# Kernel optimization log

Hardware: AMD Instinct MI355X
Metric: run time of the kernel (lower is better)

## Reference

```python
import jax, jax.numpy as jnp
import numpy as np

NODES_PER_GRAPH = 57
NUM_BRANCHES = 80
NUM_GRAPHS = 4096
IN_CH = 4
HID = 128
NUM_LAYERS = 5
BN_EPS = 1e-5


def setup_inputs() -> dict:
    key = jax.random.key(0)
    ks = jax.random.split(key, 24)
    N = NUM_GRAPHS * NODES_PER_GRAPH
    E = NUM_GRAPHS * NUM_BRANCHES * 2  # bidirectional branches per graph
    x = jax.random.normal(ks[0], (N, IN_CH), dtype=jnp.float32)
    # within-graph random edges, offset per graph block
    ep = jax.random.randint(ks[1], (2, E), 0, NODES_PER_GRAPH, dtype=jnp.int32)
    off = jnp.repeat(jnp.arange(NUM_GRAPHS, dtype=jnp.int32) * NODES_PER_GRAPH,
                     NUM_BRANCHES * 2)
    edge_index = ep + off[None, :]
    i = np.arange(NUM_BRANCHES)
    branch_u = jnp.asarray(i % NODES_PER_GRAPH, dtype=jnp.int32)
    branch_v = jnp.asarray((i * 7 + 3) % NODES_PER_GRAPH, dtype=jnp.int32)
    s = 0.05
    return {
        "x": x, "edge_index": edge_index,
        "branch_u": branch_u, "branch_v": branch_v,
        "Wp": jax.random.normal(ks[2], (IN_CH, HID)) * s,
        "bp": jnp.zeros((HID,), jnp.float32),
        "conv_W": jax.random.normal(ks[3], (NUM_LAYERS, HID, HID)) * s,
        "conv_b": jnp.zeros((NUM_LAYERS, HID), jnp.float32),
        "bn_gamma": jnp.ones((NUM_LAYERS, HID), jnp.float32),
        "bn_beta": jnp.zeros((NUM_LAYERS, HID), jnp.float32),
        "bn_mean": jax.random.normal(ks[4], (NUM_LAYERS, HID)) * 0.1,
        "bn_var": jax.random.uniform(ks[5], (NUM_LAYERS, HID)) + 0.5,
        "phys_W1": jax.random.normal(ks[6], (HID, 16)) * s,
        "phys_b1": jnp.zeros((16,), jnp.float32),
        "phys_W2": jax.random.normal(ks[7], (16, 1)) * s,
        "phys_b2": jnp.zeros((1,), jnp.float32),
        "mlp_W1": jax.random.normal(ks[8], (2 * HID + 1, HID)) * s,
        "mlp_b1": jnp.zeros((HID,), jnp.float32),
        "mlp_W2": jax.random.normal(ks[9], (HID, 1)) * s,
        "mlp_b2": jnp.zeros((1,), jnp.float32),
    }


def _gcn_conv(x, edge_index, W, b, num_nodes):
    # PyG GCNConv: add self-loops, symmetric deg^{-1/2} normalization,
    # message = norm * (x @ W)[src], scatter-add into dst, then + bias.
    h = x @ W
    loop = jnp.arange(num_nodes, dtype=edge_index.dtype)
    src = jnp.concatenate([edge_index[0], loop])
    dst = jnp.concatenate([edge_index[1], loop])
    deg = jax.ops.segment_sum(jnp.ones_like(dst, dtype=h.dtype), dst,
                              num_segments=num_nodes)  # >= 1 (self-loop)
    dinv = jax.lax.rsqrt(deg)
    norm = dinv[src] * dinv[dst]  # [E+N]
    out = jax.ops.segment_sum(h[src] * norm[:, None], dst,
                              num_segments=num_nodes)
    return out + b


def _forward(x, edge_index, branch_u, branch_v, Wp, bp, conv_W, conv_b,
             bn_gamma, bn_beta, bn_mean, bn_var, phys_W1, phys_b1, phys_W2,
             phys_b2, mlp_W1, mlp_b1, mlp_W2, mlp_b2):
    N = x.shape[0]
    num_graphs = N // NODES_PER_GRAPH
    h = x @ Wp + bp
    for l in range(NUM_LAYERS):
        res = h
        h = _gcn_conv(h, edge_index, conv_W[l], conv_b[l], N)
        # BatchNorm1d in eval mode (running stats); dropout is identity in eval
        h = (h - bn_mean[l]) * jax.lax.rsqrt(bn_var[l] + BN_EPS) * bn_gamma[l] + bn_beta[l]
        h = jax.nn.relu(h)
        h = h + res
    theta = jax.nn.relu(h @ phys_W1 + phys_b1) @ phys_W2 + phys_b2  # [N,1]
    offsets = (jnp.arange(num_graphs, dtype=jnp.int32) * NODES_PER_GRAPH)
    u_idx = (branch_u[None, :] + offsets[:, None]).reshape(-1)
    v_idx = (branch_v[None, :] + offsets[:, None]).reshape(-1)
    edge_feat = jnp.concatenate([h[u_idx], h[v_idx]], axis=-1)  # [G*80, 2H]
    delta_theta = theta[u_idx] - theta[v_idx]                   # [G*80, 1]
    comb = jnp.concatenate([edge_feat, delta_theta], axis=-1)
    return jax.nn.relu(comb @ mlp_W1 + mlp_b1) @ mlp_W2 + mlp_b2


def reference(x, edge_index, branch_u, branch_v, Wp, bp, conv_W, conv_b,
              bn_gamma, bn_beta, bn_mean, bn_var, phys_W1, phys_b1, phys_W2,
              phys_b2, mlp_W1, mlp_b1, mlp_W2, mlp_b2):
    return _forward(x, edge_index, branch_u, branch_v, Wp, bp, conv_W, conv_b,
                    bn_gamma, bn_beta, bn_mean, bn_var, phys_W1, phys_b1,
                    phys_W2, phys_b2, mlp_W1, mlp_b1, mlp_W2, mlp_b2)
```

## Files before the change

kernel.cpp:

```cpp
#include <hip/hip_runtime.h>

#define NPG 57
#define NEPG 160
#define NB 80
#define HID 128
#define NG 4096
#define NL 5

typedef __attribute__((ext_vector_type(8))) _Float16 f16x8;
typedef __attribute__((ext_vector_type(4))) _Float16 f16x4;
typedef __attribute__((ext_vector_type(4))) float f32x4;

#define MFMA16(A, B, C) __builtin_amdgcn_mfma_f32_16x16x32_f16(A, B, C, 0, 0, 0)

__device__ __forceinline__ f16x8 ldf8(const _Float16* base, int byteoff) {
    return *(const f16x8*)((const char*)base + byteoff);
}

__global__ void prep(const float* __restrict__ convW, const float* __restrict__ mlpW1,
                     const float* __restrict__ physW1, const float* __restrict__ convb,
                     const float* __restrict__ bn_gamma, const float* __restrict__ bn_beta,
                     const float* __restrict__ bn_mean, const float* __restrict__ bn_var,
                     _Float16* __restrict__ wb, float* __restrict__ fsc,
                     float* __restrict__ fsh) {
    int id = blockIdx.x * 256 + threadIdx.x;
    if (id < 114688) {
        int mat = id >> 14, rem = id & 16383, n = rem >> 7, k = rem & 127;
        float w;
        if (mat < 5)       w = convW[mat * 16384 + k * 128 + n];
        else if (mat == 5) w = mlpW1[k * 128 + n];
        else               w = mlpW1[(128 + k) * 128 + n];
        _Float16 hi = (_Float16)w;
        wb[mat * 32768 + n * 128 + k] = hi;
        wb[mat * 32768 + 16384 + n * 128 + k] = (_Float16)(w - (float)hi);
    } else if (id < 116736) {
        int p = id - 114688, n = p >> 7, k = p & 127;
        float w = physW1[k * 16 + n];
        _Float16 hi = (_Float16)w;
        wb[229376 + p] = hi;
        wb[231424 + p] = (_Float16)(w - (float)hi);
    } else if (id < 117376) {
        int p = id - 116736;
        float sc = bn_gamma[p] * rsqrtf(bn_var[p] + 1e-5f);
        fsc[p] = sc;
        fsh[p] = fmaf(convb[p] - bn_mean[p], sc, bn_beta[p]);
    }
}

__global__ __launch_bounds__(512, 2) void pinn_fused(
    const float* __restrict__ x, const int* __restrict__ edge_index,
    const int* __restrict__ branch_u, const int* __restrict__ branch_v,
    const float* __restrict__ Wp, const float* __restrict__ bp,
    const float* __restrict__ physb1, const float* __restrict__ physW2,
    const float* __restrict__ physb2,
    const float* __restrict__ mlpW1, const float* __restrict__ mlpb1,
    const float* __restrict__ mlpW2, const float* __restrict__ mlpb2,
    const _Float16* __restrict__ wb, const float* __restrict__ fsc,
    const float* __restrict__ fsh, float* __restrict__ out) {
    __shared__ _Float16 hTh[128 * 64];
    __shared__ _Float16 hTl[128 * 64];
    __shared__ _Float16 mh[64 * 128];
    __shared__ _Float16 ml[64 * 128];
    __shared__ float dinv[64];
    __shared__ int   deg[64];
    __shared__ short esrc[NEPG], edst[NEPG];
    __shared__ float theta[64];
    __shared__ float red[NB];
    __shared__ int   bu[NB], bv[NB];

    const int g = blockIdx.x;
    const int tid = threadIdx.x;
    const int lane = tid & 63;
    const int wv = tid >> 6;
    const int ln15 = lane & 15;
    const int hi4 = lane >> 4;
    const int R0 = 16 * (wv & 3);
    const int ct0 = 4 * (wv >> 2);

    float* Af = (float*)mh;
    _Float16* Ah = ml;
    _Float16* Al = ml + 4096;

    {
        int c = tid & 127;
        int sw = (c & 7) << 4;
        float w0 = Wp[c], w1 = Wp[HID + c], w2 = Wp[2 * HID + c], w3 = Wp[3 * HID + c];
        float bb = bp[c];
        for (int r = tid >> 7; r < 64; r += 4) {
            float h0 = 0.f;
            if (r < NPG) {
                float4 xv = ((const float4*)x)[g * NPG + r];
                h0 = fmaf(xv.x, w0, fmaf(xv.y, w1, fmaf(xv.z, w2, fmaf(xv.w, w3, bb))));
            }
            _Float16 hh = (_Float16)h0;
            *(_Float16*)((char*)(hTh + c * 64) + ((r * 2) ^ sw)) = hh;
            *(_Float16*)((char*)(hTl + c * 64) + ((r * 2) ^ sw)) = (_Float16)(h0 - (float)hh);
        }
    }
    for (int i = tid; i < 4096; i += 512) Af[i] = 0.f;
    if (tid < 64) deg[tid] = (tid < NPG) ? 1 : 0;
    if (tid < NB) { bu[tid] = branch_u[tid]; bv[tid] = branch_v[tid]; red[tid] = 0.f; }
    __syncthreads();

    if (tid < NEPG) {
        int gs = edge_index[g * NEPG + tid];
        int gd = edge_index[NG * NEPG + g * NEPG + tid];
        esrc[tid] = (short)(gs - g * NPG);
        edst[tid] = (short)(gd - g * NPG);
        atomicAdd(&deg[edst[tid]], 1);
    }
    __syncthreads();
    if (tid < 64) dinv[tid] = (tid < NPG) ? rsqrtf((float)deg[tid]) : 0.f;
    __syncthreads();
    if (tid < NEPG) {
        int s = esrc[tid], d = edst[tid];
        atomicAdd(&Af[d * 64 + s], dinv[s] * dinv[d]);
    }
    if (tid < NPG) atomicAdd(&Af[tid * 64 + tid], dinv[tid] * dinv[tid]);
    __syncthreads();
    for (int i = tid; i < 4096; i += 512) {
        int r = i >> 6, s = i & 63;
        float v = Af[i];
        _Float16 hi = (_Float16)v;
        int byteoff = (s * 2) ^ ((r & 7) << 4);
        *(_Float16*)((char*)(Ah + r * 64) + byteoff) = hi;
        *(_Float16*)((char*)(Al + r * 64) + byteoff) = (_Float16)(v - (float)hi);
    }
    __syncthreads();

    f16x8 Ahf[2], Alf[2];
    {
        int ar = R0 + ln15;
        int swr = (ar & 7) << 4;
        Ahf[0] = ldf8(Ah + ar * 64, ((8 * hi4) * 2) ^ swr);
        Ahf[1] = ldf8(Ah + ar * 64, ((32 + 8 * hi4) * 2) ^ swr);
        Alf[0] = ldf8(Al + ar * 64, ((8 * hi4) * 2) ^ swr);
        Alf[1] = ldf8(Al + ar * 64, ((32 + 8 * hi4) * 2) ^ swr);
    }
    __syncthreads();

    const int mrow = R0 + ln15;
    const int swm = (mrow & 7) << 4;

    for (int l = 0; l < NL; ++l) {
        f32x4 macc[4];
#pragma unroll
        for (int j = 0; j < 4; ++j) macc[j] = (f32x4){0.f, 0.f, 0.f, 0.f};
#pragma unroll
        for (int ks2 = 0; ks2 < 2; ++ks2) {
#pragma unroll
            for (int j = 0; j < 4; ++j) {
                int c = 16 * (ct0 + j) + ln15;
                int byteoff = ((32 * ks2 + 8 * hi4) * 2) ^ ((c & 7) << 4);
                f16x8 hh = ldf8(hTh + c * 64, byteoff);
                f16x8 hl = ldf8(hTl + c * 64, byteoff);
                f32x4 a = macc[j];
                a = MFMA16(Ahf[ks2], hh, a);
                a = MFMA16(Ahf[ks2], hl, a);
                a = MFMA16(Alf[ks2], hh, a);
                macc[j] = a;
            }
        }
#pragma unroll
        for (int j = 0; j < 4; ++j) {
            int c = 16 * (ct0 + j) + ln15;
#pragma unroll
            for (int q = 0; q < 4; ++q) {
                int r = R0 + 4 * hi4 + q;
                float v = macc[j][q];
                _Float16 vh = (_Float16)v;
                int byteoff = (c * 2) ^ ((r & 7) << 4);
                *(_Float16*)((char*)(mh + r * 128) + byteoff) = vh;
                *(_Float16*)((char*)(ml + r * 128) + byteoff) = (_Float16)(v - (float)vh);
            }
        }
        __syncthreads();

        const _Float16* whi = wb + 2 * l * 16384;
        const _Float16* wlo = wb + (2 * l + 1) * 16384;
        f32x4 zacc[4];
#pragma unroll
        for (int j = 0; j < 4; ++j) zacc[j] = (f32x4){0.f, 0.f, 0.f, 0.f};
#pragma unroll
        for (int ks = 0; ks < 4; ++ks) {
            int byteoff = ((32 * ks + 8 * hi4) * 2) ^ swm;
            f16x8 mhf = ldf8(mh + mrow * 128, byteoff);
            f16x8 mlf = ldf8(ml + mrow * 128, byteoff);
#pragma unroll
            for (int j = 0; j < 4; ++j) {
                int n = 16 * (ct0 + j) + ln15;
                f16x8 bh = *(const f16x8*)(whi + n * 128 + 32 * ks + 8 * hi4);
                f16x8 bl = *(const f16x8*)(wlo + n * 128 + 32 * ks + 8 * hi4);
                f32x4 a = zacc[j];
                a = MFMA16(mhf, bh, a);
                a = MFMA16(mhf, bl, a);
                a = MFMA16(mlf, bh, a);
                zacc[j] = a;
            }
        }

        if (l < NL - 1) {
#pragma unroll
            for (int j = 0; j < 4; ++j) {
                int c = 16 * (ct0 + j) + ln15;
                float scv = fsc[l * HID + c], shv = fsh[l * HID + c];
                int byteoff = ((R0 + 4 * hi4) * 2) ^ ((c & 7) << 4);
                f16x4 rh = *(const f16x4*)((const char*)(hTh + c * 64) + byteoff);
                f16x4 rl = *(const f16x4*)((const char*)(hTl + c * 64) + byteoff);
                f16x4 nh, nl;
#pragma unroll
                for (int q = 0; q < 4; ++q) {
                    float hold = (float)rh[q] + (float)rl[q];
                    float hnew = fmaxf(fmaf(zacc[j][q], scv, shv), 0.f) + hold;
                    _Float16 vh = (_Float16)hnew;
                    nh[q] = vh;
                    nl[q] = (_Float16)(hnew - (float)vh);
                }
                *(f16x4*)((char*)(hTh + c * 64) + byteoff) = nh;
                *(f16x4*)((char*)(hTl + c * 64) + byteoff) = nl;
            }
            __syncthreads();
        } else {
            __syncthreads();
#pragma unroll
            for (int j = 0; j < 4; ++j) {
                int c = 16 * (ct0 + j) + ln15;
                float scv = fsc[l * HID + c], shv = fsh[l * HID + c];
                int tbyte = ((R0 + 4 * hi4) * 2) ^ ((c & 7) << 4);
                f16x4 rh = *(const f16x4*)((const char*)(hTh + c * 64) + tbyte);
                f16x4 rl = *(const f16x4*)((const char*)(hTl + c * 64) + tbyte);
#pragma unroll
                for (int q = 0; q < 4; ++q) {
                    int r = R0 + 4 * hi4 + q;
                    float hold = (float)rh[q] + (float)rl[q];
                    float hnew = fmaxf(fmaf(zacc[j][q], scv, shv), 0.f) + hold;
                    _Float16 vh = (_Float16)hnew;
                    int byteoff = (c * 2) ^ ((r & 7) << 4);
                    *(_Float16*)((char*)(mh + r * 128) + byteoff) = vh;
                    *(_Float16*)((char*)(ml + r * 128) + byteoff) = (_Float16)(hnew - (float)vh);
                }
            }
            __syncthreads();
        }
    }

    if (wv < 4) {
        f32x4 t4 = (f32x4){0.f, 0.f, 0.f, 0.f};
        int r = 16 * wv + ln15;
        int swr = (r & 7) << 4;
#pragma unroll
        for (int ks = 0; ks < 4; ++ks) {
            int byteoff = ((32 * ks + 8 * hi4) * 2) ^ swr;
            f16x8 fh = ldf8(mh + r * 128, byteoff);
            f16x8 fl = ldf8(ml + r * 128, byteoff);
            f16x8 bh = *(const f16x8*)(wb + 229376 + ln15 * 128 + 32 * ks + 8 * hi4);
            f16x8 bl = *(const f16x8*)(wb + 231424 + ln15 * 128 + 32 * ks + 8 * hi4);
            t4 = MFMA16(fh, bh, t4);
            t4 = MFMA16(fh, bl, t4);
            t4 = MFMA16(fl, bh, t4);
        }
        float b1 = physb1[ln15], w2 = physW2[ln15], b2 = physb2[0];
#pragma unroll
        for (int q = 0; q < 4; ++q) {
            float val = fmaxf(t4[q] + b1, 0.f) * w2;
#pragma unroll
            for (int o = 1; o < 16; o <<= 1) val += __shfl_xor(val, o, 16);
            int rq = 16 * wv + 4 * hi4 + q;
            if (ln15 == 0 && rq < NPG) theta[rq] = val + b2;
        }
    }
    __syncthreads();

    for (int task = wv; task < 10; task += 8) {
        int t = task >> 1;
        int cb = 4 * (task & 1);
        int b = 16 * t + ln15;
        int ru = bu[b], rv = bv[b];
        f32x4 acc4[4];
#pragma unroll
        for (int j = 0; j < 4; ++j) acc4[j] = (f32x4){0.f, 0.f, 0.f, 0.f};
        const _Float16* ph = wb + 10 * 16384;
        const _Float16* pl = wb + 11 * 16384;
        const _Float16* qh = wb + 12 * 16384;
        const _Float16* ql = wb + 13 * 16384;
#pragma unroll
        for (int ks = 0; ks < 4; ++ks) {
            int ko = 32 * ks + 8 * hi4;
            f16x8 uh = ldf8(mh + ru * 128, ((ko * 2) ^ ((ru & 7) << 4)));
            f16x8 ul = ldf8(ml + ru * 128, ((ko * 2) ^ ((ru & 7) << 4)));
#pragma unroll
            for (int j = 0; j < 4; ++j) {
                int n = 16 * (cb + j) + ln15;
                f16x8 bh = *(const f16x8*)(ph + n * 128 + ko);
                f16x8 bl = *(const f16x8*)(pl + n * 128 + ko);
                f32x4 a = acc4[j];
                a = MFMA16(uh, bh, a);
                a = MFMA16(uh, bl, a);
                a = MFMA16(ul, bh, a);
                acc4[j] = a;
            }
            f16x8 vh = ldf8(mh + rv * 128, ((ko * 2) ^ ((rv & 7) << 4)));
            f16x8 vl = ldf8(ml + rv * 128, ((ko * 2) ^ ((rv & 7) << 4)));
#pragma unroll
            for (int j = 0; j < 4; ++j) {
                int n = 16 * (cb + j) + ln15;
                f16x8 bh = *(const f16x8*)(qh + n * 128 + ko);
                f16x8 bl = *(const f16x8*)(ql + n * 128 + ko);
                f32x4 a = acc4[j];
                a = MFMA16(vh, bh, a);
                a = MFMA16(vh, bl, a);
                a = MFMA16(vl, bh, a);
                acc4[j] = a;
            }
        }
        float dth[4];
#pragma unroll
        for (int q = 0; q < 4; ++q) {
            int bb = 16 * t + 4 * hi4 + q;
            dth[q] = theta[bu[bb]] - theta[bv[bb]];
        }
        float sums[4] = {0.f, 0.f, 0.f, 0.f};
#pragma unroll
        for (int j = 0; j < 4; ++j) {
            int ch = 16 * (cb + j) + ln15;
            float w256 = mlpW1[256 * HID + ch];
            float b1 = mlpb1[ch];
            float w2 = mlpW2[ch];
#pragma unroll
            for (int q = 0; q < 4; ++q)
                sums[q] += fmaxf(fmaf(dth[q], w256, acc4[j][q] + b1), 0.f) * w2;
        }
#pragma unroll
        for (int q = 0; q < 4; ++q) {
#pragma unroll
            for (int o = 1; o < 16; o <<= 1) sums[q] += __shfl_xor(sums[q], o, 16);
            if (ln15 == 0) atomicAdd(&red[16 * t + 4 * hi4 + q], sums[q]);
        }
    }
    __syncthreads();
    if (tid < NB) out[g * NB + tid] = red[tid] + mlpb2[0];
}

extern "C" void kernel_launch(void* const* d_in, const int* in_sizes, int n_in,
                              void* d_out, int out_size, void* d_ws, size_t ws_size,
                              hipStream_t stream) {
    const float* x          = (const float*)d_in[0];
    const int*   edge_index = (const int*)d_in[1];
    const int*   branch_u   = (const int*)d_in[2];
    const int*   branch_v   = (const int*)d_in[3];
    const float* Wp         = (const float*)d_in[4];
    const float* bp         = (const float*)d_in[5];
    const float* convW      = (const float*)d_in[6];
    const float* convb      = (const float*)d_in[7];
    const float* bn_gamma   = (const float*)d_in[8];
    const float* bn_beta    = (const float*)d_in[9];
    const float* bn_mean    = (const float*)d_in[10];
    const float* bn_var     = (const float*)d_in[11];
    const float* physW1     = (const float*)d_in[12];
    const float* physb1     = (const float*)d_in[13];
    const float* physW2     = (const float*)d_in[14];
    const float* physb2     = (const float*)d_in[15];
    const float* mlpW1      = (const float*)d_in[16];
    const float* mlpb1      = (const float*)d_in[17];
    const float* mlpW2      = (const float*)d_in[18];
    const float* mlpb2      = (const float*)d_in[19];
    float* out = (float*)d_out;

    _Float16* wb = (_Float16*)d_ws;
    float* fsc = (float*)((char*)d_ws + 466944);
    float* fsh = fsc + 640;

    prep<<<459, 256, 0, stream>>>(convW, mlpW1, physW1, convb,
                                  bn_gamma, bn_beta, bn_mean, bn_var, wb, fsc, fsh);
    pinn_fused<<<NG, 512, 0, stream>>>(
        x, edge_index, branch_u, branch_v, Wp, bp,
        physb1, physW2, physb2, mlpW1, mlpb1, mlpW2, mlpb2,
        wb, fsc, fsh, out);
}
```

Measured before the change: 1.223 ms.

## Drop low-half of aggregated features and reuse hTl buffer to cut LDS

Removes the separate ml shared buffer: the aggregated A·h result is stored only as a single fp16 value, and the mlf correction MFMA in the weight GEMM is dropped. The adjacency hi/lo split is now computed directly from the fp32 Af into registers instead of going through an LDS staging pass and an extra barrier. The final-layer low residual is written into the now-dead hTl region after a barrier. This reduces LDS footprint (possibly raising occupancy), MFMA count and synchronisation, at the cost of lower precision in the aggregated features.

Result: faster. 1.185 ms (-3.1%).

```diff
diff --git a/kernel.cpp b/kernel.cpp
--- a/kernel.cpp
+++ b/kernel.cpp
@@ -60,7 +60,6 @@
     __shared__ _Float16 hTh[128 * 64];
     __shared__ _Float16 hTl[128 * 64];
     __shared__ _Float16 mh[64 * 128];
-    __shared__ _Float16 ml[64 * 128];
     __shared__ float dinv[64];
     __shared__ int   deg[64];
     __shared__ short esrc[NEPG], edst[NEPG];
@@ -78,8 +77,7 @@
     const int ct0 = 4 * (wv >> 2);
 
     float* Af = (float*)mh;
-    _Float16* Ah = ml;
-    _Float16* Al = ml + 4096;
+    _Float16* hrl = hTl;
 
     {
         int c = tid & 127;
@@ -118,24 +116,25 @@
     }
     if (tid < NPG) atomicAdd(&Af[tid * 64 + tid], dinv[tid] * dinv[tid]);
     __syncthreads();
-    for (int i = tid; i < 4096; i += 512) {
-        int r = i >> 6, s = i & 63;
-        float v = Af[i];
-        _Float16 hi = (_Float16)v;
-        int byteoff = (s * 2) ^ ((r & 7) << 4);
-        *(_Float16*)((char*)(Ah + r * 64) + byteoff) = hi;
-        *(_Float16*)((char*)(Al + r * 64) + byteoff) = (_Float16)(v - (float)hi);
-    }
-    __syncthreads();
 
     f16x8 Ahf[2], Alf[2];
     {
         int ar = R0 + ln15;
-        int swr = (ar & 7) << 4;
-        Ahf[0] = ldf8(Ah + ar * 64, ((8 * hi4) * 2) ^ swr);
-        Ahf[1] = ldf8(Ah + ar * 64, ((32 + 8 * hi4) * 2) ^ swr);
-        Alf[0] = ldf8(Al + ar * 64, ((8 * hi4) * 2) ^ swr);
-        Alf[1] = ldf8(Al + ar * 64, ((32 + 8 * hi4) * 2) ^ swr);
+#define CVTE(V, I, FH, FL) { _Float16 t_ = (_Float16)(V); FH[I] = t_; FL[I] = (_Float16)((V) - (float)t_); }
+#pragma unroll
+        for (int ks2 = 0; ks2 < 2; ++ks2) {
+            const float* ap = &Af[ar * 64 + 32 * ks2 + 8 * hi4];
+            float4 a0 = *(const float4*)ap;
+            float4 a1 = *(const float4*)(ap + 4);
+            f16x8 fh, fl;
+            CVTE(a0.x, 0, fh, fl) CVTE(a0.y, 1, fh, fl)
+            CVTE(a0.z, 2, fh, fl) CVTE(a0.w, 3, fh, fl)
+            CVTE(a1.x, 4, fh, fl) CVTE(a1.y, 5, fh, fl)
+            CVTE(a1.z, 6, fh, fl) CVTE(a1.w, 7, fh, fl)
+            Ahf[ks2] = fh;
+            Alf[ks2] = fl;
+        }
+#undef CVTE
     }
     __syncthreads();
 
@@ -167,11 +166,8 @@
 #pragma unroll
             for (int q = 0; q < 4; ++q) {
                 int r = R0 + 4 * hi4 + q;
-                float v = macc[j][q];
-                _Float16 vh = (_Float16)v;
-                int byteoff = (c * 2) ^ ((r & 7) << 4);
-                *(_Float16*)((char*)(mh + r * 128) + byteoff) = vh;
-                *(_Float16*)((char*)(ml + r * 128) + byteoff) = (_Float16)(v - (float)vh);
+                *(_Float16*)((char*)(mh + r * 128) + ((c * 2) ^ ((r & 7) << 4))) =
+                    (_Float16)macc[j][q];
             }
         }
         __syncthreads();
@@ -185,7 +181,6 @@
         for (int ks = 0; ks < 4; ++ks) {
             int byteoff = ((32 * ks + 8 * hi4) * 2) ^ swm;
             f16x8 mhf = ldf8(mh + mrow * 128, byteoff);
-            f16x8 mlf = ldf8(ml + mrow * 128, byteoff);
 #pragma unroll
             for (int j = 0; j < 4; ++j) {
                 int n = 16 * (ct0 + j) + ln15;
@@ -194,7 +189,6 @@
                 f32x4 a = zacc[j];
                 a = MFMA16(mhf, bh, a);
                 a = MFMA16(mhf, bl, a);
-                a = MFMA16(mlf, bh, a);
                 zacc[j] = a;
             }
         }
@@ -221,23 +215,34 @@
             }
             __syncthreads();
         } else {
-            __syncthreads();
+            f32x4 hn[4];
 #pragma unroll
             for (int j = 0; j < 4; ++j) {
                 int c = 16 * (ct0 + j) + ln15;
                 float scv = fsc[l * HID + c], shv = fsh[l * HID + c];
-                int tbyte = ((R0 + 4 * hi4) * 2) ^ ((c & 7) << 4);
-                f16x4 rh = *(const f16x4*)((const char*)(hTh + c * 64) + tbyte);
-                f16x4 rl = *(const f16x4*)((const char*)(hTl + c * 64) + tbyte);
+                int byteoff = ((R0 + 4 * hi4) * 2) ^ ((c & 7) << 4);
+                f16x4 rh = *(const f16x4*)((const char*)(hTh + c * 64) + byteoff);
+                f16x4 rl = *(const f16x4*)((const char*)(hTl + c * 64) + byteoff);
+                f32x4 t;
+#pragma unroll
+                for (int q = 0; q < 4; ++q) {
+                    float hold = (float)rh[q] + (float)rl[q];
+                    t[q] = fmaxf(fmaf(zacc[j][q], scv, shv), 0.f) + hold;
+                }
+                hn[j] = t;
+            }
+            __syncthreads();
+#pragma unroll
+            for (int j = 0; j < 4; ++j) {
+                int c = 16 * (ct0 + j) + ln15;
 #pragma unroll
                 for (int q = 0; q < 4; ++q) {
                     int r = R0 + 4 * hi4 + q;
-                    float hold = (float)rh[q] + (float)rl[q];
-                    float hnew = fmaxf(fmaf(zacc[j][q], scv, shv), 0.f) + hold;
-                    _Float16 vh = (_Float16)hnew;
+                    float v = hn[j][q];
+                    _Float16 vh = (_Float16)v;
                     int byteoff = (c * 2) ^ ((r & 7) << 4);
                     *(_Float16*)((char*)(mh + r * 128) + byteoff) = vh;
-                    *(_Float16*)((char*)(ml + r * 128) + byteoff) = (_Float16)(hnew - (float)vh);
+                    *(_Float16*)((char*)(hrl + r * 128) + byteoff) = (_Float16)(v - (float)vh);
                 }
             }
             __syncthreads();
@@ -252,7 +257,7 @@
         for (int ks = 0; ks < 4; ++ks) {
             int byteoff = ((32 * ks + 8 * hi4) * 2) ^ swr;
             f16x8 fh = ldf8(mh + r * 128, byteoff);
-            f16x8 fl = ldf8(ml + r * 128, byteoff);
+            f16x8 fl = ldf8(hrl + r * 128, byteoff);
             f16x8 bh = *(const f16x8*)(wb + 229376 + ln15 * 128 + 32 * ks + 8 * hi4);
             f16x8 bl = *(const f16x8*)(wb + 231424 + ln15 * 128 + 32 * ks + 8 * hi4);
             t4 = MFMA16(fh, bh, t4);
@@ -287,7 +292,7 @@
         for (int ks = 0; ks < 4; ++ks) {
             int ko = 32 * ks + 8 * hi4;
             f16x8 uh = ldf8(mh + ru * 128, ((ko * 2) ^ ((ru & 7) << 4)));
-            f16x8 ul = ldf8(ml + ru * 128, ((ko * 2) ^ ((ru & 7) << 4)));
+            f16x8 ul = ldf8(hrl + ru * 128, ((ko * 2) ^ ((ru & 7) << 4)));
 #pragma unroll
             for (int j = 0; j < 4; ++j) {
                 int n = 16 * (cb + j) + ln15;
@@ -300,7 +305,7 @@
                 acc4[j] = a;
             }
             f16x8 vh = ldf8(mh + rv * 128, ((ko * 2) ^ ((rv & 7) << 4)));
-            f16x8 vl = ldf8(ml + rv * 128, ((ko * 2) ^ ((rv & 7) << 4)));
+            f16x8 vl = ldf8(hrl + rv * 128, ((ko * 2) ^ ((rv & 7) << 4)));
 #pragma unroll
             for (int j = 0; j < 4; ++j) {
                 int n = 16 * (cb + j) + ln15;
```
